# Performance work log

Hardware: AMD Instinct MI355X
Metric: run time of the kernel (lower is better)

Reference implementation:

```python
import jax, jax.numpy as jnp
import numpy as np

B, N, F_IN, F_OUT, D = 8, 2048, 256, 128, 3
ALPHA = 0.2       # leaky relu slope
CUT_OFF = 0.1     # distance gate sharpness
NEG_INF = -9e15


def setup_inputs() -> dict:
    key = jax.random.key(0)
    k1, k2, k3, k4 = jax.random.split(key, 4)
    x = jax.random.normal(k1, (B, N, F_IN), dtype=jnp.float32)
    coord = jax.random.normal(k2, (B, N, D), dtype=jnp.float32)
    # xavier_uniform-style scale (gain=1.414); normal init is fine for a reference
    w_std = 1.414 * np.sqrt(2.0 / (F_IN + F_OUT))
    a_std = 1.414 * np.sqrt(2.0 / (2 * F_OUT + 1))
    W = jax.random.normal(k3, (F_IN, F_OUT), dtype=jnp.float32) * w_std
    a = jax.random.normal(k4, (2 * F_OUT, 1), dtype=jnp.float32) * a_std
    return {"x": x, "coord": coord, "W": W, "a": a}


def reference(x, coord, W, a):
    # h: [B, N, F_OUT]
    h = jnp.matmul(x, W)
    # The original builds a_input=[h_i || h_j] and does a_input @ a.
    # Equivalent: e_ij = leaky_relu(h_i @ a[:F] + h_j @ a[F:]).
    f_src = jnp.matmul(h, a[:F_OUT])   # [B, N, 1]
    f_dst = jnp.matmul(h, a[F_OUT:])   # [B, N, 1]
    e = f_src + jnp.swapaxes(f_dst, 1, 2)            # [B, N, N]
    e = jnp.where(e > 0, e, ALPHA * e)               # leaky relu
    # pairwise squared distances -> exponential gate
    diff = coord[:, :, None, :] - coord[:, None, :, :]   # [B, N, N, D]
    loc = jnp.exp(-CUT_OFF * jnp.sum(diff * diff, axis=-1))  # [B, N, N]
    att_logits = jnp.where(loc > 0.01, e * loc, NEG_INF)
    attention = jax.nn.softmax(att_logits, axis=2)
    # dropout is identity in eval mode
    h_prime = jnp.matmul(attention, h)               # [B, N, F_OUT]
    return jax.nn.elu(h_prime)                       # concat=True path
```

## Files before the change

### kernel.cpp

```cpp
#include <hip/hip_runtime.h>
#include <hip/hip_bf16.h>

#define B_    8
#define N_    2048
#define FIN_  256
#define FOUT_ 128
#define NROWS (B_*N_)

typedef __attribute__((ext_vector_type(8))) short short8;
typedef __attribute__((ext_vector_type(4))) float f32x4;

__device__ __forceinline__ float bf2f(unsigned short u) {
  return __uint_as_float(((unsigned int)u) << 16);
}
__device__ __forceinline__ unsigned short f2bf(float f) {
  unsigned int u = __float_as_uint(f);
  u += 0x7FFFu + ((u >> 16) & 1u);
  return (unsigned short)(u >> 16);
}
__device__ __forceinline__ float ldin(const void* p, size_t idx, int isbf) {
  if (isbf) return bf2f(((const unsigned short*)p)[idx]);
  return ((const float*)p)[idx];
}
__device__ __forceinline__ unsigned pk2bf(float a, float b) {
  return (unsigned)f2bf(a) | ((unsigned)f2bf(b) << 16);
}
__device__ __forceinline__ float ex2(float x) {
#if __has_builtin(__builtin_amdgcn_exp2f)
  return __builtin_amdgcn_exp2f(x);
#else
  return __expf(x * 0.69314718056f);
#endif
}
__device__ __forceinline__ unsigned encf(float f) {
  unsigned u = __float_as_uint(f);
  return (u & 0x80000000u) ? ~u : (u | 0x80000000u);
}
__device__ __forceinline__ float decf(unsigned k) {
  return (k & 0x80000000u) ? __uint_as_float(k ^ 0x80000000u) : __uint_as_float(~k);
}
__device__ __forceinline__ int detect_bf(const void* x, int* cnt) {
  const unsigned short* u = (const unsigned short*)x;
  int c = 0;
  for (int i = threadIdx.x; i < 8192; i += 256) {
    unsigned short v = u[i];
    int e = (v >> 7) & 0xFF;
    if ((e >= 110 && e <= 145) || (v & 0x7FFF) == 0) c++;
  }
  cnt[threadIdx.x] = c;
  __syncthreads();
  for (int s = 128; s > 0; s >>= 1) {
    if (threadIdx.x < s) cnt[threadIdx.x] += cnt[threadIdx.x + s];
    __syncthreads();
  }
  return cnt[0] > 7373;
}

__global__ __launch_bounds__(256)
void k_prep(const void* __restrict__ x, const void* __restrict__ W,
            const void* __restrict__ a,
            unsigned short* __restrict__ WT, float* __restrict__ wa,
            int* __restrict__ flag, unsigned* __restrict__ MdstE) {
  __shared__ int cnt[256];
  const int isbf = detect_bf(x, cnt);
  if (blockIdx.x < 128) {
    int f = blockIdx.x, k = threadIdx.x;
    WT[f * 256 + k] = f2bf(ldin(W, (size_t)k * 128 + f, isbf));
  } else {
    __shared__ float as_s[256];
    int k = threadIdx.x;
    as_s[k] = ldin(a, k, isbf);
    __syncthreads();
    float s = 0.f, d = 0.f;
    for (int f = 0; f < 128; f++) {
      float w = ldin(W, (size_t)k * 128 + f, isbf);
      s += w * as_s[f];
      d += w * as_s[128 + f];
    }
    wa[k] = s;
    wa[256 + k] = d;
    if (k == 0) *flag = isbf;
    if (k < 8) MdstE[k * 32] = 0u;
  }
}

__global__ __launch_bounds__(256)
void k_h(const void* __restrict__ x, const void* __restrict__ coord,
         const unsigned short* __restrict__ WT,
         const float* __restrict__ wa, const int* __restrict__ flag,
         unsigned short* __restrict__ hT, float* __restrict__ fsrc,
         float4* __restrict__ cpack, unsigned* __restrict__ MdstE) {
  __shared__ __align__(16) unsigned short xs[32][264];
  __shared__ float wa_s[512];
  __shared__ float mxs[8];
  const int isbf = *flag;
  const int t    = threadIdx.x;
  const int row0 = blockIdx.x * 32;

  wa_s[t] = wa[t];
  wa_s[256 + t] = wa[256 + t];
  __syncthreads();

  const int c = t & 31;
  float sp[4], dp[4];
  if (isbf) {
    const unsigned short* xu = (const unsigned short*)x;
#pragma unroll
    for (int u = 0; u < 4; u++) {
      int r = u * 8 + (t >> 5);
      short8 sh = *(const short8*)&xu[(size_t)(row0 + r) * FIN_ + c * 8];
      *(short8*)&xs[r][c * 8] = sh;
      float s = 0.f, d = 0.f;
#pragma unroll
      for (int e = 0; e < 8; e++) {
        float xv = bf2f((unsigned short)sh[e]);
        s += xv * wa_s[c * 8 + e];
        d += xv * wa_s[256 + c * 8 + e];
      }
      sp[u] = s; dp[u] = d;
    }
  } else {
    const float* xf = (const float*)x;
#pragma unroll
    for (int u = 0; u < 4; u++) {
      int r = u * 8 + (t >> 5);
      float4 v0 = *(const float4*)&xf[(size_t)(row0 + r) * FIN_ + c * 8];
      float4 v1 = *(const float4*)&xf[(size_t)(row0 + r) * FIN_ + c * 8 + 4];
      float vv[8] = {v0.x, v0.y, v0.z, v0.w, v1.x, v1.y, v1.z, v1.w};
      short8 sh;
      float s = 0.f, d = 0.f;
#pragma unroll
      for (int e = 0; e < 8; e++) {
        sh[e] = (short)f2bf(vv[e]);
        s += vv[e] * wa_s[c * 8 + e];
        d += vv[e] * wa_s[256 + c * 8 + e];
      }
      *(short8*)&xs[r][c * 8] = sh;
      sp[u] = s; dp[u] = d;
    }
  }
#pragma unroll
  for (int off = 16; off >= 1; off >>= 1) {
#pragma unroll
    for (int u = 0; u < 4; u++) {
      sp[u] += __shfl_xor(sp[u], off, 64);
      dp[u] += __shfl_xor(dp[u], off, 64);
    }
  }
  if (c == 0) {
    float lm = -1e30f;
#pragma unroll
    for (int u = 0; u < 4; u++) {
      int r = u * 8 + (t >> 5);
      size_t rg = (size_t)(row0 + r);
      fsrc[rg] = sp[u];
      cpack[rg] = make_float4(ldin(coord, rg * 3 + 0, isbf),
                              ldin(coord, rg * 3 + 1, isbf),
                              ldin(coord, rg * 3 + 2, isbf),
                              dp[u] * 1.44269504f);
      lm = fmaxf(lm, dp[u]);
    }
    mxs[t >> 5] = lm;
  }
  __syncthreads();
  if (t == 0) {
    float m8 = mxs[0];
#pragma unroll
    for (int i = 1; i < 8; i++) m8 = fmaxf(m8, mxs[i]);
    atomicMax(&MdstE[(row0 >> 11) * 32], encf(m8));
  }

  const int lane = t & 63, w = t >> 6;
  const int m = lane & 15, quad = lane >> 4;
  const int slab = w >> 1, fh = w & 1;

  f32x4 acc[4];
#pragma unroll
  for (int i = 0; i < 4; i++) acc[i] = (f32x4){0.f, 0.f, 0.f, 0.f};

#pragma unroll
  for (int ks = 0; ks < 8; ks++) {
    short8 ah = *(const short8*)&xs[slab * 16 + m][ks * 32 + quad * 8];
#pragma unroll
    for (int ft = 0; ft < 4; ft++) {
      int f = fh * 64 + ft * 16 + m;
      short8 bh = *(const short8*)&WT[(size_t)f * 256 + ks * 32 + quad * 8];
      acc[ft] = __builtin_amdgcn_mfma_f32_16x16x32_bf16(ah, bh, acc[ft], 0, 0, 0);
    }
  }

  size_t n0 = (size_t)blockIdx.x * 2 + slab;
  unsigned short* hblk = hT + n0 * (FOUT_ * 16);
#pragma unroll
  for (int ft = 0; ft < 4; ft++) {
    int f = fh * 64 + ft * 16 + m;
    int jo = (quad * 4) ^ (((f >> 2) & 1) << 3);
    *(uint2*)&hblk[f * 16 + jo] = make_uint2(
        pk2bf(acc[ft][0], acc[ft][1]), pk2bf(acc[ft][2], acc[ft][3]));
  }
}

__global__ __launch_bounds__(1024, 4)
void k_attn(const unsigned short* __restrict__ hT, const float4* __restrict__ cpack,
            const float* __restrict__ fsrc, const unsigned* __restrict__ MdstE,
            const int* __restrict__ flag, void* __restrict__ out) {
  const int isbf = *flag;
  const int tid = threadIdx.x;
  const int b   = blockIdx.x >> 5;
  const int q0  = (blockIdx.x & 31) * 64;

  __shared__ __align__(16) uint4 ldsBu[2][2048];
  __shared__ __align__(16) unsigned short phi[2][64][136];
  __shared__ __align__(16) float4 cjs[2][144];
  __shared__ float denomS[64];

  const int qA   = tid >> 4;
  const int jseg = tid & 15;
  const size_t qglb = (size_t)b * N_ + q0 + qA;
  const float4 cq  = cpack[qglb];
  const float  fsq = fsrc[qglb];
  const float  fsqL = fsq * 1.44269504f;
  const float  mBqL = -fmaxf(0.f, fsq + decf(MdstE[b * 32])) * 1.44269504f;

  const int lane = tid & 63, w = tid >> 6;
  const int m = lane & 15, quad = lane >> 4;
  const int qg = w & 3, fg = w >> 2;
  const int hsel = (quad & 1) ^ ((m >> 2) & 1);

  f32x4 acc[2], accD;
  acc[0] = (f32x4){0.f, 0.f, 0.f, 0.f};
  acc[1] = (f32x4){0.f, 0.f, 0.f, 0.f};
  accD   = (f32x4){0.f, 0.f, 0.f, 0.f};
  const short8 bones = {(short)0x3F80, (short)0x3F80, (short)0x3F80, (short)0x3F80,
                        (short)0x3F80, (short)0x3F80, (short)0x3F80, (short)0x3F80};

  const unsigned short* hTb = hT + (size_t)b * (N_ * FOUT_);
  const uint4* gB = (const uint4*)hTb;
  const float4* cpb = cpack + (size_t)b * N_;

  auto logits = [&](int tt, unsigned* pk) {
    const float4* cb = cjs[tt & 1];
#pragma unroll
    for (int jp = 0; jp < 4; jp++) {
      const int j0 = jseg * 8 + 2 * jp;
      const int ix = j0 + (j0 >> 3);
      const float4 cj0 = cb[ix];
      const float4 cj1 = cb[ix + 1];
      float dx0 = cq.x - cj0.x, dy0 = cq.y - cj0.y, dz0 = cq.z - cj0.z;
      float dx1 = cq.x - cj1.x, dy1 = cq.y - cj1.y, dz1 = cq.z - cj1.z;
      float d20 = fmaf(dz0, dz0, fmaf(dy0, dy0, dx0 * dx0));
      float d21 = fmaf(dz1, dz1, fmaf(dy1, dy1, dx1 * dx1));
      float loc0 = ex2(-0.14426950408f * d20);
      float loc1 = ex2(-0.14426950408f * d21);
      float xL0 = fsqL + cj0.w, xL1 = fsqL + cj1.w;
      float eL0 = fmaxf(xL0, 0.2f * xL0);
      float eL1 = fmaxf(xL1, 0.2f * xL1);
      float p0 = ex2(fmaf(eL0, loc0, mBqL));
      float p1 = ex2(fmaf(eL1, loc1, mBqL));
      p0 = (d20 < 46.0517f) ? p0 : 0.f;
      p1 = (d21 < 46.0517f) ? p1 : 0.f;
      unsigned r;
      asm("v_cvt_pk_bf16_f32 %0, %1, %2" : "=v"(r) : "v"(p0), "v"(p1));
      pk[jp] = r;
    }
  };

  auto store_phi = [&](int tt, const unsigned* pk) {
    *(uint4*)&phi[tt & 1][qA][jseg * 8] =
        make_uint4(pk[0], pk[1], pk[2], pk[3]);
  };

  auto mfma_tile = [&](int tb) {
    const unsigned short* pb = &phi[tb][qg * 16 + m][0];
    const unsigned short* bb = (const unsigned short*)ldsBu[tb];
#pragma unroll
    for (int ks = 0; ks < 4; ks++) {
      short8 ah = *(const short8*)&pb[ks * 32 + quad * 8];
      if (fg == 0)
        accD = __builtin_amdgcn_mfma_f32_16x16x32_bf16(ah, bones, accD, 0, 0, 0);
#pragma unroll
      for (int ft = 0; ft < 2; ft++) {
        const int f = fg * 32 + ft * 16 + m;
        const short8 bh = *(const short8*)
            &bb[(ks * 2 + (quad >> 1)) * 2048 + f * 16 + hsel * 8];
        acc[ft] = __builtin_amdgcn_mfma_f32_16x16x32_bf16(ah, bh, acc[ft], 0, 0, 0);
      }
    }
  };

  if (tid < 256) {
    const int tile = tid >> 7, j = tid & 127;
    cjs[tile][j + (j >> 3)] = cpb[tid];
  }
  {
    uint4 pv[2];
#pragma unroll
    for (int k = 0; k < 2; k++) pv[k] = gB[k * 1024 + tid];
#pragma unroll
    for (int k = 0; k < 2; k++) ldsBu[0][k * 1024 + tid] = pv[k];
  }
  __syncthreads();
  {
    unsigned pk0[4];
    logits(0, pk0);
    store_phi(0, pk0);
  }
  __syncthreads();

  const int jr = tid & 127;
  for (int t = 0; t < 16; t++) {
    uint4 bv[2];
    if (t < 15) {
#pragma unroll
      for (int k = 0; k < 2; k++)
        bv[k] = gB[(size_t)(t + 1) * 2048 + k * 1024 + tid];
    }
    float4 cg;
    if (t < 14 && tid < 128) cg = cpb[(t + 2) * 128 + jr];

    unsigned pk[4];
    if (t < 15) logits(t + 1, pk);

    mfma_tile(t & 1);

    if (t < 15) {
#pragma unroll
      for (int k = 0; k < 2; k++)
        ldsBu[(t + 1) & 1][k * 1024 + tid] = bv[k];
      store_phi(t + 1, pk);
    }
    if (t < 14 && tid < 128) cjs[t & 1][jr + (jr >> 3)] = cg;
    __syncthreads();
  }

  if (fg == 0 && m == 0) {
#pragma unroll
    for (int r = 0; r < 4; r++) denomS[qg * 16 + quad * 4 + r] = accD[r];
  }
  __syncthreads();
#pragma unroll
  for (int ft = 0; ft < 2; ft++) {
    const int f = fg * 32 + ft * 16 + m;
#pragma unroll
    for (int r = 0; r < 4; r++) {
      const int q = qg * 16 + quad * 4 + r;
      float v = acc[ft][r] / fmaxf(denomS[q], 1e-30f);
      v = (v > 0.f) ? v : (__expf(v) - 1.0f);
      size_t oidx = ((size_t)(b * N_ + q0 + q)) * FOUT_ + f;
      if (isbf) ((unsigned short*)out)[oidx] = f2bf(v);
      else      ((float*)out)[oidx] = v;
    }
  }
}

extern "C" void kernel_launch(void* const* d_in, const int* in_sizes, int n_in,
                              void* d_out, int out_size, void* d_ws, size_t ws_size,
                              hipStream_t stream) {
  const void* x     = d_in[0];
  const void* coord = d_in[1];
  const void* W     = d_in[2];
  const void* a     = d_in[3];

  int*            flag  = (int*)d_ws;
  unsigned*       MdstE = (unsigned*)d_ws + 64;
  unsigned short* hT    = (unsigned short*)((float*)d_ws + 512);
  unsigned short* WT    = hT + (size_t)NROWS * FOUT_;
  float*          wa    = (float*)(WT + 128 * 256);
  float*          fsrc  = wa + 512;
  float4*         cpack = (float4*)(fsrc + NROWS);

  k_prep<<<129, 256, 0, stream>>>(x, W, a, WT, wa, flag, MdstE);
  k_h   <<<NROWS / 32, 256, 0, stream>>>(x, coord, WT, wa, flag, hT, fsrc, cpack, MdstE);
  k_attn<<<B_ * (N_ / 64), 1024, 0, stream>>>(hT, cpack, fsrc, MdstE, flag, d_out);
}
```

Baseline: 137.2 us.

## Split MFMA work over key slices and compute softmax denominator with scalar sums

Warps in the attention kernel now each own one feature group and one 32-wide slice of the key dimension, rather than one query group. Each warp loads its B fragments once per tile and reuses them across four query subtiles, which cuts repeated LDS reads of B. The softmax denominator MFMA against a ones matrix is replaced by per-thread sums of the rounded bf16 probabilities, reduced with shuffles. The price is four times more accumulator registers and a three-step cross-warp reduction through LDS at the end.

```diff
diff --git a/kernel.cpp b/kernel.cpp
--- a/kernel.cpp
+++ b/kernel.cpp
@@ -221,18 +221,18 @@
   const float  fsq = fsrc[qglb];
   const float  fsqL = fsq * 1.44269504f;
   const float  mBqL = -fmaxf(0.f, fsq + decf(MdstE[b * 32])) * 1.44269504f;
+  float ds = 0.f;
 
   const int lane = tid & 63, w = tid >> 6;
   const int m = lane & 15, quad = lane >> 4;
-  const int qg = w & 3, fg = w >> 2;
+  const int fg = w & 3, js = w >> 2;
   const int hsel = (quad & 1) ^ ((m >> 2) & 1);
 
-  f32x4 acc[2], accD;
-  acc[0] = (f32x4){0.f, 0.f, 0.f, 0.f};
-  acc[1] = (f32x4){0.f, 0.f, 0.f, 0.f};
-  accD   = (f32x4){0.f, 0.f, 0.f, 0.f};
-  const short8 bones = {(short)0x3F80, (short)0x3F80, (short)0x3F80, (short)0x3F80,
-                        (short)0x3F80, (short)0x3F80, (short)0x3F80, (short)0x3F80};
+  f32x4 acc[4][2];
+#pragma unroll
+  for (int i = 0; i < 4; i++)
+#pragma unroll
+    for (int j = 0; j < 2; j++) acc[i][j] = (f32x4){0.f, 0.f, 0.f, 0.f};
 
   const unsigned short* hTb = hT + (size_t)b * (N_ * FOUT_);
   const uint4* gB = (const uint4*)hTb;
@@ -263,6 +263,10 @@
       asm("v_cvt_pk_bf16_f32 %0, %1, %2" : "=v"(r) : "v"(p0), "v"(p1));
       pk[jp] = r;
     }
+#pragma unroll
+    for (int jp = 0; jp < 4; jp++)
+      ds += bf2f((unsigned short)(pk[jp] & 0xFFFF)) +
+            bf2f((unsigned short)(pk[jp] >> 16));
   };
 
   auto store_phi = [&](int tt, const unsigned* pk) {
@@ -271,20 +275,17 @@
   };
 
   auto mfma_tile = [&](int tb) {
-    const unsigned short* pb = &phi[tb][qg * 16 + m][0];
     const unsigned short* bb = (const unsigned short*)ldsBu[tb];
-#pragma unroll
-    for (int ks = 0; ks < 4; ks++) {
-      short8 ah = *(const short8*)&pb[ks * 32 + quad * 8];
-      if (fg == 0)
-        accD = __builtin_amdgcn_mfma_f32_16x16x32_bf16(ah, bones, accD, 0, 0, 0);
-#pragma unroll
-      for (int ft = 0; ft < 2; ft++) {
-        const int f = fg * 32 + ft * 16 + m;
-        const short8 bh = *(const short8*)
-            &bb[(ks * 2 + (quad >> 1)) * 2048 + f * 16 + hsel * 8];
-        acc[ft] = __builtin_amdgcn_mfma_f32_16x16x32_bf16(ah, bh, acc[ft], 0, 0, 0);
-      }
+    const int f0 = fg * 32 + m;
+    const short8 bh0 = *(const short8*)
+        &bb[(js * 2 + (quad >> 1)) * 2048 + f0 * 16 + hsel * 8];
+    const short8 bh1 = *(const short8*)
+        &bb[(js * 2 + (quad >> 1)) * 2048 + (f0 + 16) * 16 + hsel * 8];
+#pragma unroll
+    for (int qt = 0; qt < 4; qt++) {
+      short8 ah = *(const short8*)&phi[tb][qt * 16 + m][js * 32 + quad * 8];
+      acc[qt][0] = __builtin_amdgcn_mfma_f32_16x16x32_bf16(ah, bh0, acc[qt][0], 0, 0, 0);
+      acc[qt][1] = __builtin_amdgcn_mfma_f32_16x16x32_bf16(ah, bh1, acc[qt][1], 0, 0, 0);
     }
   };
 
@@ -333,22 +334,52 @@
     __syncthreads();
   }
 
-  if (fg == 0 && m == 0) {
-#pragma unroll
-    for (int r = 0; r < 4; r++) denomS[qg * 16 + quad * 4 + r] = accD[r];
-  }
-  __syncthreads();
-#pragma unroll
-  for (int ft = 0; ft < 2; ft++) {
-    const int f = fg * 32 + ft * 16 + m;
-#pragma unroll
-    for (int r = 0; r < 4; r++) {
-      const int q = qg * 16 + quad * 4 + r;
-      float v = acc[ft][r] / fmaxf(denomS[q], 1e-30f);
-      v = (v > 0.f) ? v : (__expf(v) - 1.0f);
-      size_t oidx = ((size_t)(b * N_ + q0 + q)) * FOUT_ + f;
-      if (isbf) ((unsigned short*)out)[oidx] = f2bf(v);
-      else      ((float*)out)[oidx] = v;
+#pragma unroll
+  for (int off = 1; off <= 8; off <<= 1) ds += __shfl_xor(ds, off, 64);
+  if (jseg == 0) denomS[qA] = ds;
+
+  f32x4* xv = (f32x4*)ldsBu;
+  auto writeSlot = [&](int slot) {
+#pragma unroll
+    for (int qt = 0; qt < 4; qt++)
+#pragma unroll
+      for (int ft = 0; ft < 2; ft++) {
+        const int i = qt * 2 + ft;
+        xv[slot * 512 + lane * 8 + (i ^ (lane & 7))] = acc[qt][ft];
+      }
+  };
+  auto readSlot = [&](int slot) {
+#pragma unroll
+    for (int qt = 0; qt < 4; qt++)
+#pragma unroll
+      for (int ft = 0; ft < 2; ft++) {
+        const int i = qt * 2 + ft;
+        acc[qt][ft] += xv[slot * 512 + lane * 8 + (i ^ (lane & 7))];
+      }
+  };
+  if (js & 1) writeSlot(fg * 2 + (js >> 1));
+  __syncthreads();
+  if (!(js & 1)) readSlot(fg * 2 + (js >> 1));
+  __syncthreads();
+  if (js == 2) writeSlot(fg);
+  __syncthreads();
+
+  if (js == 0) {
+    readSlot(fg);
+#pragma unroll
+    for (int ft = 0; ft < 2; ft++) {
+      const int f = fg * 32 + ft * 16 + m;
+#pragma unroll
+      for (int qt = 0; qt < 4; qt++)
+#pragma unroll
+        for (int r = 0; r < 4; r++) {
+          const int q = qt * 16 + quad * 4 + r;
+          float v = acc[qt][ft][r] / fmaxf(denomS[q], 1e-30f);
+          v = (v > 0.f) ? v : (__expf(v) - 1.0f);
+          size_t oidx = ((size_t)(b * N_ + q0 + q)) * FOUT_ + f;
+          if (isbf) ((unsigned short*)out)[oidx] = f2bf(v);
+          else      ((float*)out)[oidx] = v;
+        }
     }
   }
 }
```

After: 132.1 us (median of 2 runs). -3.7%, faster.
